# Kernel optimization log

Hardware: AMD Instinct MI355X
Metric: run time of the kernel (lower is better)

## Reference

```python
import jax, jax.numpy as jnp
import numpy as np

K = 2          # neighbors per point (init default k=2)
ALPHA = 5e-4   # regularization weight (init default)
N_CLASSES = 1000


def setup_inputs() -> dict:
    key = jax.random.key(0)
    k1, k2, k3 = jax.random.split(key, 3)
    n, d_feat, n_cls = 4096, 1024, N_CLASSES
    x_batch = jax.random.normal(k1, (n, d_feat), dtype=jnp.float32)
    y_batch = jax.random.randint(k2, (n,), 0, n_cls, dtype=jnp.int32)
    y_output = jax.random.normal(k3, (n, n_cls), dtype=jnp.float32)
    return {"x_batch": x_batch, "y_batch": y_batch, "y_output": y_output}


def _pairwise_dist(a):
    # ||a_i - a_j|| via gram trick; clamp for numerical safety.
    sq = jnp.sum(a * a, axis=-1)                       # [n]
    d2 = sq[:, None] + sq[None, :] - 2.0 * (a @ a.T)   # [n, n]
    d2 = jnp.maximum(d2, 0.0)
    # sqrt with zero-safe gradient (diag / coincident points)
    safe = jnp.where(d2 > 0.0, d2, 1.0)
    return jnp.where(d2 > 0.0, jnp.sqrt(safe), 0.0)


def reference(x_batch, y_batch, y_output):
    n = x_batch.shape[0]
    d = _pairwise_dist(x_batch)                        # [n, n] input-space distances

    # K nearest neighbors, excluding self (i != j in the original loops)
    d_knn = d + jnp.where(jnp.eye(n, dtype=bool), jnp.inf, 0.0)
    _, nbr_idx = jax.lax.top_k(-d_knn, K)              # [n, K] smallest distances
    nbr_mask = jnp.zeros((n, n), dtype=d.dtype)
    nbr_mask = nbr_mask.at[jnp.arange(n)[:, None], nbr_idx].set(1.0)

    same_class = (y_batch[:, None] == y_batch[None, :])
    w = jnp.exp(-d) * nbr_mask                         # exp(-d) on KNN edges only
    # w_diff = w_int - w_pen: +exp(-d) for same-class neighbors, -exp(-d) otherwise
    w_diff = jnp.where(same_class, w, -w)

    y_norm = _pairwise_dist(y_output)                  # [n, n] ||y_out_i - y_out_j||
    reg_value = jnp.sum(w_diff * y_norm)
    return ALPHA * reg_value
```

## Files before the change

kernel.cpp:

```cpp
#include <hip/hip_runtime.h>
#include <math.h>

#define ALPHA 5e-4f
#define BIG 1e30f

typedef __attribute__((ext_vector_type(4))) float f32x4;

__device__ __forceinline__ void gload16(const void* g, void* l) {
    __builtin_amdgcn_global_load_lds(
        (const __attribute__((address_space(1))) void*)g,
        (__attribute__((address_space(3))) void*)l, 16, 0, 0);
}

__global__ __launch_bounds__(256)
void conv_fp8_kernel(const float* __restrict__ X, unsigned char* __restrict__ Xq,
                     float* __restrict__ sqn32, int d) {
    const int w = threadIdx.x >> 6, lane = threadIdx.x & 63;
    const int row = blockIdx.x * 4 + w;
    const float4* src = reinterpret_cast<const float4*>(X + (size_t)row * d);
    int4* dst = reinterpret_cast<int4*>(Xq + (size_t)row * d);
    float s = 0.f;
    const int ng = d >> 4;
    for (int g = lane; g < ng; g += 64) {
        int wds[4];
#pragma unroll
        for (int q = 0; q < 4; ++q) {
            float4 v = src[g * 4 + q];
            s += v.x * v.x + v.y * v.y + v.z * v.z + v.w * v.w;
            int t0 = __builtin_amdgcn_cvt_pk_fp8_f32(v.x, v.y, 0, false);
            wds[q] = __builtin_amdgcn_cvt_pk_fp8_f32(v.z, v.w, t0, true);
        }
        dst[g] = make_int4(wds[0], wds[1], wds[2], wds[3]);
    }
    for (int off = 1; off < 64; off <<= 1) s += __shfl_xor(s, off, 64);
    if (lane == 0) sqn32[row] = s;
}

#define BMQ 256
#define TKB 64

__global__ __launch_bounds__(512)
void gram_top2_mfma(const unsigned char* __restrict__ Xq, const float* __restrict__ sqn,
                    float* __restrict__ cand_s, int* __restrict__ cand_i,
                    int n, int d, int nbc, int cpx) {
    __shared__ unsigned char As[4][BMQ * TKB];
    __shared__ unsigned char Bs[4][BMQ * TKB];

    const int bid = blockIdx.x;
    const int swz = (bid & 7) * cpx + (bid >> 3);
    const int rb = swz >> 4, cb = swz & 15;

    const int row0 = rb * BMQ, col0 = cb * BMQ;
    const int t = threadIdx.x;
    const int w = t >> 6, l = t & 63;
    const int wr = w >> 2, wcn = w & 3;
    const int lc = l & 15, lg = l >> 4;

    f32x4 acc[8][4];
#pragma unroll
    for (int i = 0; i < 8; ++i)
#pragma unroll
        for (int j = 0; j < 4; ++j) acc[i][j] = (f32x4){0.f, 0.f, 0.f, 0.f};

    const int srow = w * 16 + (l >> 2);
    const int sblk = ((l & 3) ^ ((l >> 3) & 3)) << 4;
    const size_t gA0 = (size_t)(row0 + srow) * d + sblk;
    const size_t gB0 = (size_t)(col0 + srow) * d + sblk;
    const size_t hstep = (size_t)128 * d;
    const int wb = w * 1024;

    const int nt = d / TKB;

#define STAGE_A(bi, ks)                                                   \
    {                                                                     \
        const size_t ko = (size_t)(ks) * TKB;                             \
        gload16(Xq + gA0 + ko, As[bi] + wb);                              \
        gload16(Xq + gA0 + ko + hstep, As[bi] + wb + 8192);               \
    }
#define STAGE_B(bi, ks)                                                   \
    {                                                                     \
        const size_t ko = (size_t)(ks) * TKB;                             \
        gload16(Xq + gB0 + ko, Bs[bi] + wb);                              \
        gload16(Xq + gB0 + ko + hstep, Bs[bi] + wb + 8192);               \
    }

    STAGE_A(0, 0) STAGE_B(0, 0)
    STAGE_A(1, 1) STAGE_B(1, 1)
    STAGE_A(2, 2) STAGE_B(2, 2)
    asm volatile("s_waitcnt vmcnt(8)" ::: "memory");
    __builtin_amdgcn_s_barrier();

    const int csw = ((lc >> 1) & 3) << 1;

    for (int ks = 0; ks < nt; ++ks) {
        const int bi = ks & 3;
        const int sb = (ks + 3) & 3;
        const bool st = (ks + 3) < nt;

#pragma unroll
        for (int ww = 0; ww < 2; ++ww) {
            long long a[8], b[4];
            const int ch = ((ww * 4 + lg) ^ csw) * 8;
#pragma unroll
            for (int mi = 0; mi < 8; ++mi)
                a[mi] = *reinterpret_cast<const long long*>(
                    &As[bi][(wr * 128 + mi * 16 + lc) * TKB + ch]);
#pragma unroll
            for (int ni = 0; ni < 4; ++ni)
                b[ni] = *reinterpret_cast<const long long*>(
                    &Bs[bi][(wcn * 64 + ni * 16 + lc) * TKB + ch]);

            if (st) {
                if (ww == 0) { STAGE_A(sb, ks + 3) }
                else         { STAGE_B(sb, ks + 3) }
            }
            __builtin_amdgcn_s_barrier();

            __builtin_amdgcn_s_setprio(1);
#pragma unroll
            for (int mi = 0; mi < 8; ++mi)
#pragma unroll
                for (int ni = 0; ni < 4; ++ni)
                    acc[mi][ni] = __builtin_amdgcn_mfma_f32_16x16x32_fp8_fp8(
                        a[mi], b[ni], acc[mi][ni], 0, 0, 0);
            __builtin_amdgcn_s_setprio(0);

            if (ww == 1) {
                if (ks <= nt - 4) {
                    asm volatile("s_waitcnt vmcnt(8)" ::: "memory");
                } else if (ks == nt - 3) {
                    asm volatile("s_waitcnt vmcnt(4)" ::: "memory");
                } else if (ks == nt - 2) {
                    asm volatile("s_waitcnt vmcnt(0)" ::: "memory");
                }
            }
            __builtin_amdgcn_s_barrier();
        }
    }
#undef STAGE_A
#undef STAGE_B

    float sq_c[4];
#pragma unroll
    for (int ni = 0; ni < 4; ++ni) sq_c[ni] = sqn[col0 + wcn * 64 + ni * 16 + lc];
    const int strip_r = cb * 4 + wcn;

#pragma unroll
    for (int mi = 0; mi < 8; ++mi) {
#pragma unroll
        for (int j = 0; j < 4; ++j) {
            const int grow = row0 + wr * 128 + mi * 16 + lg * 4 + j;
            float s1v = BIG, s2v = BIG;
            int i1 = -1, i2 = -1;
#pragma unroll
            for (int ni = 0; ni < 4; ++ni) {
                const int gcol = col0 + wcn * 64 + ni * 16 + lc;
                float s = sq_c[ni] - 2.f * acc[mi][ni][j];
                if (gcol == grow) s = BIG;
                if (s < s1v) { s2v = s1v; i2 = i1; s1v = s; i1 = gcol; }
                else if (s < s2v) { s2v = s; i2 = gcol; }
            }
            for (int off = 1; off < 16; off <<= 1) {
                float b1 = __shfl_xor(s1v, off, 16);
                int  bi1 = __shfl_xor(i1, off, 16);
                float b2 = __shfl_xor(s2v, off, 16);
                int  bi2 = __shfl_xor(i2, off, 16);
                if (b1 < s1v) { s2v = s1v; i2 = i1; s1v = b1; i1 = bi1; }
                else if (b1 < s2v) { s2v = b1; i2 = bi1; }
                if (b2 < s2v) { s2v = b2; i2 = bi2; }
            }
            if (lc == 0) {
                size_t base = ((size_t)grow * 64 + strip_r) * 2;
                cand_s[base] = s1v; cand_s[base + 1] = s2v;
                cand_i[base] = i1; cand_i[base + 1] = i2;
            }
        }
    }
}

__global__ __launch_bounds__(256)
void merge_edges_kernel(const float* __restrict__ sqn,
                        const float* __restrict__ cand_s, const int* __restrict__ cand_i,
                        const int* __restrict__ yb, const float* __restrict__ yo,
                        float* __restrict__ partial, int ncls) {
    const int w = threadIdx.x >> 6, lane = threadIdx.x & 63;
    const int row = blockIdx.x * 4 + w;

    float2 cs = reinterpret_cast<const float2*>(cand_s + (size_t)row * 128)[lane];
    int2   ci = reinterpret_cast<const int2*>(cand_i + (size_t)row * 128)[lane];
    float s1 = cs.x, s2 = cs.y;
    int i1 = ci.x, i2 = ci.y;
    if (s2 < s1) { float ts = s1; s1 = s2; s2 = ts; int ti = i1; i1 = i2; i2 = ti; }

    for (int off = 1; off < 64; off <<= 1) {
        float b1 = __shfl_xor(s1, off, 64);
        int  bi1 = __shfl_xor(i1, off, 64);
        float b2 = __shfl_xor(s2, off, 64);
        int  bi2 = __shfl_xor(i2, off, 64);
        if (b1 < s1) { s2 = s1; i2 = i1; s1 = b1; i1 = bi1; }
        else if (b1 < s2) { s2 = b1; i2 = bi1; }
        if (b2 < s2) { s2 = b2; i2 = bi2; }
    }
    const int yr = yb[row];
    const float sr = sqn[row];
    float w1 = ((yr == yb[i1]) ? 1.f : -1.f) * expf(-sqrtf(fmaxf(sr + s1, 0.f)));
    float w2 = ((yr == yb[i2]) ? 1.f : -1.f) * expf(-sqrtf(fmaxf(sr + s2, 0.f)));

    const float4* yr4 = reinterpret_cast<const float4*>(yo + (size_t)row * ncls);
    const float4* y14 = reinterpret_cast<const float4*>(yo + (size_t)i1 * ncls);
    const float4* y24 = reinterpret_cast<const float4*>(yo + (size_t)i2 * ncls);
    const int nv4 = ncls >> 2;
    float a1 = 0.f, a2 = 0.f;
    for (int c = lane; c < nv4; c += 64) {
        float4 v = yr4[c];
        float4 u1 = y14[c];
        float4 u2 = y24[c];
        float tx = v.x - u1.x, ty = v.y - u1.y, tz = v.z - u1.z, tw = v.w - u1.w;
        a1 = fmaf(tx, tx, fmaf(ty, ty, fmaf(tz, tz, fmaf(tw, tw, a1))));
        tx = v.x - u2.x; ty = v.y - u2.y; tz = v.z - u2.z; tw = v.w - u2.w;
        a2 = fmaf(tx, tx, fmaf(ty, ty, fmaf(tz, tz, fmaf(tw, tw, a2))));
    }
    for (int c = (nv4 << 2) + lane; c < ncls; c += 64) {
        float v = yo[(size_t)row * ncls + c];
        float t1 = v - yo[(size_t)i1 * ncls + c];
        float t2 = v - yo[(size_t)i2 * ncls + c];
        a1 = fmaf(t1, t1, a1);
        a2 = fmaf(t2, t2, a2);
    }
    for (int off = 1; off < 64; off <<= 1) {
        a1 += __shfl_xor(a1, off, 64);
        a2 += __shfl_xor(a2, off, 64);
    }
    if (lane == 0)
        partial[row] = w1 * sqrtf(a1) + w2 * sqrtf(a2);
}

__global__ __launch_bounds__(256)
void final_reduce_kernel(const float* __restrict__ partial, float* __restrict__ out, int n) {
    const int t = threadIdx.x;
    __shared__ float red[4];
    float s = 0.f;
    const int nv4 = n >> 2;
    const float4* p4 = reinterpret_cast<const float4*>(partial);
    for (int c = t; c < nv4; c += 256) {
        float4 v = p4[c];
        s += v.x + v.y + v.z + v.w;
    }
    for (int off = 1; off < 64; off <<= 1) s += __shfl_xor(s, off, 64);
    if ((t & 63) == 0) red[t >> 6] = s;
    __syncthreads();
    if (t == 0) out[0] = ALPHA * (red[0] + red[1] + red[2] + red[3]);
}

extern "C" void kernel_launch(void* const* d_in, const int* in_sizes, int n_in,
                              void* d_out, int out_size, void* d_ws, size_t ws_size,
                              hipStream_t stream) {
    const float* X  = (const float*)d_in[0];
    const int*   yb = (const int*)d_in[1];
    const float* yo = (const float*)d_in[2];
    float* out = (float*)d_out;

    const int n    = in_sizes[1];
    const int d    = in_sizes[0] / n;
    const int ncls = in_sizes[2] / n;
    const int nbc  = n / BMQ;

    char* wsb = (char*)d_ws;
    size_t off = 0;
    float* sqn32 = (float*)(wsb + off);         off += ((size_t)n * 4 + 255) & ~(size_t)255;
    unsigned char* Xq = (unsigned char*)(wsb + off); off += ((size_t)n * d + 255) & ~(size_t)255;
    float* cand_s = (float*)(wsb + off);        off += ((size_t)n * 64 * 2 * 4 + 255) & ~(size_t)255;
    int*   cand_i = (int*)(wsb + off);          off += ((size_t)n * 64 * 2 * 4 + 255) & ~(size_t)255;
    float* partial = (float*)(wsb + off);

    conv_fp8_kernel<<<n / 4, 256, 0, stream>>>(X, Xq, sqn32, d);

    const int nsq = nbc * nbc;
    const int cpx = nsq / 8;
    gram_top2_mfma<<<nsq, 512, 0, stream>>>(Xq, sqn32, cand_s, cand_i, n, d, nbc, cpx);

    merge_edges_kernel<<<n / 4, 256, 0, stream>>>(sqn32, cand_s, cand_i, yb, yo, partial, ncls);

    final_reduce_kernel<<<1, 256, 0, stream>>>(partial, out, n);
}
```

Baseline: 66.73 us.

## Restructure fp8 gram mainloop into 3-stage ring with 16-byte LDS fragment reads

Cuts the LDS staging ring in the fp8 gram/top-2 kernel from four buffers to three and the prefetch depth from three tiles to two. The inner loop is split into four phases, each with one global-to-LDS load. Fragments are now read as 16-byte vectors covering both k-halves, with a new XOR swizzle. This lowers LDS use, which may allow more resident blocks and cuts LDS read instructions, but the shallower prefetch and extra barriers per tile may expose more memory latency.

After: 62.51 us. -6.3%, faster.

```diff
diff --git a/kernel.cpp b/kernel.cpp
--- a/kernel.cpp
+++ b/kernel.cpp
@@ -5,6 +5,7 @@
 #define BIG 1e30f
 
 typedef __attribute__((ext_vector_type(4))) float f32x4;
+typedef __attribute__((ext_vector_type(2))) long long llx2;
 
 __device__ __forceinline__ void gload16(const void* g, void* l) {
     __builtin_amdgcn_global_load_lds(
@@ -43,8 +44,8 @@
 void gram_top2_mfma(const unsigned char* __restrict__ Xq, const float* __restrict__ sqn,
                     float* __restrict__ cand_s, int* __restrict__ cand_i,
                     int n, int d, int nbc, int cpx) {
-    __shared__ unsigned char As[4][BMQ * TKB];
-    __shared__ unsigned char Bs[4][BMQ * TKB];
+    __shared__ unsigned char As[3][BMQ * TKB];
+    __shared__ unsigned char Bs[3][BMQ * TKB];
 
     const int bid = blockIdx.x;
     const int swz = (bid & 7) * cpx + (bid >> 3);
@@ -62,83 +63,78 @@
 #pragma unroll
         for (int j = 0; j < 4; ++j) acc[i][j] = (f32x4){0.f, 0.f, 0.f, 0.f};
 
-    const int srow = w * 16 + (l >> 2);
-    const int sblk = ((l & 3) ^ ((l >> 3) & 3)) << 4;
-    const size_t gA0 = (size_t)(row0 + srow) * d + sblk;
-    const size_t gB0 = (size_t)(col0 + srow) * d + sblk;
+    const int sblk = ((t & 3) ^ ((t >> 3) & 3)) << 4;
+    const size_t gA0 = (size_t)(row0 + (t >> 2)) * d + sblk;
+    const size_t gB0 = (size_t)(col0 + (t >> 2)) * d + sblk;
     const size_t hstep = (size_t)128 * d;
     const int wb = w * 1024;
 
     const int nt = d / TKB;
-
-#define STAGE_A(bi, ks)                                                   \
-    {                                                                     \
-        const size_t ko = (size_t)(ks) * TKB;                             \
-        gload16(Xq + gA0 + ko, As[bi] + wb);                              \
-        gload16(Xq + gA0 + ko + hstep, As[bi] + wb + 8192);               \
-    }
-#define STAGE_B(bi, ks)                                                   \
-    {                                                                     \
-        const size_t ko = (size_t)(ks) * TKB;                             \
-        gload16(Xq + gB0 + ko, Bs[bi] + wb);                              \
-        gload16(Xq + gB0 + ko + hstep, Bs[bi] + wb + 8192);               \
-    }
-
-    STAGE_A(0, 0) STAGE_B(0, 0)
-    STAGE_A(1, 1) STAGE_B(1, 1)
-    STAGE_A(2, 2) STAGE_B(2, 2)
-    asm volatile("s_waitcnt vmcnt(8)" ::: "memory");
+    const int rblk = (lg ^ ((lc >> 1) & 3)) << 4;
+
+#pragma unroll
+    for (int s = 0; s < 2; ++s) {
+        const size_t ko = (size_t)s * TKB;
+        gload16(Xq + gA0 + ko,         As[s] + wb);
+        gload16(Xq + gA0 + ko + hstep, As[s] + 8192 + wb);
+        gload16(Xq + gB0 + ko,         Bs[s] + wb);
+        gload16(Xq + gB0 + ko + hstep, Bs[s] + 8192 + wb);
+    }
+    asm volatile("s_waitcnt vmcnt(4)" ::: "memory");
     __builtin_amdgcn_s_barrier();
 
-    const int csw = ((lc >> 1) & 3) << 1;
-
+    int r0 = 0, r1 = 1, r2 = 2;
     for (int ks = 0; ks < nt; ++ks) {
-        const int bi = ks & 3;
-        const int sb = (ks + 3) & 3;
-        const bool st = (ks + 3) < nt;
-
-#pragma unroll
-        for (int ww = 0; ww < 2; ++ww) {
-            long long a[8], b[4];
-            const int ch = ((ww * 4 + lg) ^ csw) * 8;
-#pragma unroll
-            for (int mi = 0; mi < 8; ++mi)
-                a[mi] = *reinterpret_cast<const long long*>(
-                    &As[bi][(wr * 128 + mi * 16 + lc) * TKB + ch]);
-#pragma unroll
-            for (int ni = 0; ni < 4; ++ni)
-                b[ni] = *reinterpret_cast<const long long*>(
-                    &Bs[bi][(wcn * 64 + ni * 16 + lc) * TKB + ch]);
+        const unsigned char* Ab = As[r0];
+        const unsigned char* Bb = Bs[r0];
+        const bool st = (ks + 2) < nt;
+        const size_t ko2 = (size_t)(ks + 2) * TKB;
+        llx2 bf[4];
+
+#pragma unroll
+        for (int p = 0; p < 4; ++p) {
+            if (p == 0) {
+#pragma unroll
+                for (int ni = 0; ni < 4; ++ni)
+                    bf[ni] = *reinterpret_cast<const llx2*>(
+                        Bb + (wcn * 64 + ni * 16 + lc) * 64 + rblk);
+            }
+            llx2 af[2];
+#pragma unroll
+            for (int q = 0; q < 2; ++q)
+                af[q] = *reinterpret_cast<const llx2*>(
+                    Ab + (wr * 128 + (p * 2 + q) * 16 + lc) * 64 + rblk);
 
             if (st) {
-                if (ww == 0) { STAGE_A(sb, ks + 3) }
-                else         { STAGE_B(sb, ks + 3) }
+                if (p == 0)      gload16(Xq + gA0 + ko2,         As[r2] + wb);
+                else if (p == 1) gload16(Xq + gA0 + ko2 + hstep, As[r2] + 8192 + wb);
+                else if (p == 2) gload16(Xq + gB0 + ko2,         Bs[r2] + wb);
+                else             gload16(Xq + gB0 + ko2 + hstep, Bs[r2] + 8192 + wb);
             }
             __builtin_amdgcn_s_barrier();
 
             __builtin_amdgcn_s_setprio(1);
 #pragma unroll
-            for (int mi = 0; mi < 8; ++mi)
-#pragma unroll
-                for (int ni = 0; ni < 4; ++ni)
+            for (int q = 0; q < 2; ++q) {
+                const int mi = p * 2 + q;
+#pragma unroll
+                for (int ni = 0; ni < 4; ++ni) {
                     acc[mi][ni] = __builtin_amdgcn_mfma_f32_16x16x32_fp8_fp8(
-                        a[mi], b[ni], acc[mi][ni], 0, 0, 0);
+                        af[q].x, bf[ni].x, acc[mi][ni], 0, 0, 0);
+                    acc[mi][ni] = __builtin_amdgcn_mfma_f32_16x16x32_fp8_fp8(
+                        af[q].y, bf[ni].y, acc[mi][ni], 0, 0, 0);
+                }
+            }
             __builtin_amdgcn_s_setprio(0);
 
-            if (ww == 1) {
-                if (ks <= nt - 4) {
-                    asm volatile("s_waitcnt vmcnt(8)" ::: "memory");
-                } else if (ks == nt - 3) {
-                    asm volatile("s_waitcnt vmcnt(4)" ::: "memory");
-                } else if (ks == nt - 2) {
-                    asm volatile("s_waitcnt vmcnt(0)" ::: "memory");
-                }
+            if (p == 3) {
+                if (st) { asm volatile("s_waitcnt vmcnt(4)" ::: "memory"); }
+                else    { asm volatile("s_waitcnt vmcnt(0)" ::: "memory"); }
             }
             __builtin_amdgcn_s_barrier();
         }
-    }
-#undef STAGE_A
-#undef STAGE_B
+        int tmp = r0; r0 = r1; r1 = r2; r2 = tmp;
+    }
 
     float sq_c[4];
 #pragma unroll
```
